# Performance work log

Hardware: AMD Instinct MI355X
Metric: run time of the kernel (lower is better)

The kernel has to match this reference:

```python
import jax, jax.numpy as jnp
import numpy as np

EPS = 1e-6
N_HEADS = 16
N_KV_HEADS = 4
HEAD_DIM = 128
DIM = 2048
SEQ = 2048
BATCH = 2


def _make_freqs_cis(seqlen, head_dim, theta=10000.0):
    inv = 1.0 / (theta ** (jnp.arange(0, head_dim, 2, dtype=jnp.float32) / head_dim))  # [hd/2]
    t = jnp.arange(seqlen, dtype=jnp.float32)
    ang = jnp.outer(t, inv)  # [seq, hd/2]
    return jnp.stack([jnp.cos(ang), jnp.sin(ang)], axis=-1)  # [seq, hd/2, 2]


def setup_inputs() -> dict:
    key = jax.random.key(0)
    k1, k2, k3 = jax.random.split(key, 3)
    std = 0.02
    x = jax.random.normal(k1, (BATCH, SEQ, DIM), dtype=jnp.float32)
    freqs_cis = _make_freqs_cis(SEQ, HEAD_DIM)
    norm_w = jnp.ones((DIM,), dtype=jnp.float32)
    wqkv_w = jax.random.normal(k2, ((N_HEADS + 2 * N_KV_HEADS) * HEAD_DIM, DIM), dtype=jnp.float32) * std
    wo_w = jax.random.normal(k3, (DIM, N_HEADS * HEAD_DIM), dtype=jnp.float32) * std
    return {"x": x, "freqs_cis": freqs_cis, "norm_w": norm_w, "wqkv_w": wqkv_w, "wo_w": wo_w}


def _rope(t, cos, sin):
    # t: [b, s, h, hd] viewed as pairs; cos/sin: [s, hd/2]
    b, s, h, hd = t.shape
    tr = t.reshape(b, s, h, hd // 2, 2)
    xr, xi = tr[..., 0], tr[..., 1]
    c = cos[None, :, None, :]
    sn = sin[None, :, None, :]
    out_r = xr * c - xi * sn
    out_i = xr * sn + xi * c
    return jnp.stack([out_r, out_i], axis=-1).reshape(b, s, h, hd)


def reference(x, freqs_cis, norm_w, wqkv_w, wo_w):
    bs, seqlen, dim = x.shape
    n_rep = N_HEADS // N_KV_HEADS
    # RMSNorm
    xn = x * jax.lax.rsqrt(jnp.mean(x * x, axis=-1, keepdims=True) + EPS) * norm_w
    # fused QKV projection
    qkv = jnp.einsum('bsd,ed->bse', xn, wqkv_w)
    q_sz = N_HEADS * HEAD_DIM
    kv_sz = N_KV_HEADS * HEAD_DIM
    xq = qkv[..., :q_sz].reshape(bs, seqlen, N_HEADS, HEAD_DIM)
    xk = qkv[..., q_sz:q_sz + kv_sz].reshape(bs, seqlen, N_KV_HEADS, HEAD_DIM)
    xv = qkv[..., q_sz + kv_sz:].reshape(bs, seqlen, N_KV_HEADS, HEAD_DIM)
    cos, sin = freqs_cis[..., 0], freqs_cis[..., 1]
    xq = _rope(xq, cos, sin)
    xk = _rope(xk, cos, sin)
    # GQA: group q heads so kv broadcast replaces repeat_kv materialization
    q = xq.transpose(0, 2, 1, 3).reshape(bs, N_KV_HEADS, n_rep, seqlen, HEAD_DIM)
    k = xk.transpose(0, 2, 1, 3)  # [b, g, s, d]
    v = xv.transpose(0, 2, 1, 3)
    scale = 1.0 / jnp.sqrt(jnp.float32(HEAD_DIM))
    scores = jnp.einsum('bgrqd,bgkd->bgrqk', q, k) * scale
    causal = jnp.tril(jnp.ones((seqlen, seqlen), dtype=bool))
    scores = jnp.where(causal, scores, jnp.finfo(scores.dtype).min)
    probs = jax.nn.softmax(scores, axis=-1)
    out = jnp.einsum('bgrqk,bgkd->bgrqd', probs, v)
    out = out.reshape(bs, N_HEADS, seqlen, HEAD_DIM).transpose(0, 2, 1, 3).reshape(bs, seqlen, N_HEADS * HEAD_DIM)
    return jnp.einsum('bse,de->bsd', out, wo_w)
```

## Files before the change

### kernel.cpp

```cpp
#include <hip/hip_runtime.h>
#include <cstdint>
#include <cstddef>

typedef __bf16 bhalf;
typedef __bf16 bhalf8 __attribute__((ext_vector_type(8)));
typedef __bf16 bhalf4 __attribute__((ext_vector_type(4)));
typedef float f32x4 __attribute__((ext_vector_type(4)));
typedef float f32x16 __attribute__((ext_vector_type(16)));

#define RMS_EPS 1e-6f
#define N_HEADS 16
#define N_KV 4
#define HD 128
#define DIM 2048
#define SEQ 2048
#define BATCH 2

static __device__ __forceinline__ f32x4 mfma16(bhalf8 a, bhalf8 b, f32x4 c) {
    return __builtin_amdgcn_mfma_f32_16x16x32_bf16(a, b, c, 0, 0, 0);
}
static __device__ __forceinline__ f32x16 mfma32(bhalf8 a, bhalf8 b, f32x16 c) {
    return __builtin_amdgcn_mfma_f32_32x32x16_bf16(a, b, c, 0, 0, 0);
}

static __device__ __forceinline__ void gload16(const bhalf* g, bhalf* l) {
    __builtin_amdgcn_global_load_lds((const __attribute__((address_space(1))) unsigned int*)g,
                                     (__attribute__((address_space(3))) unsigned int*)l,
                                     16, 0, 0);
}

static __device__ __forceinline__ unsigned cvt_pk_bf16(float a, float b) {
    unsigned r;
    asm volatile("v_cvt_pk_bf16_f32 %0, %1, %2" : "=v"(r) : "v"(a), "v"(b));
    return r;
}
static __device__ __forceinline__ void plane32_swap(unsigned& a, unsigned& b) {
    asm volatile("v_permlane32_swap_b32 %0, %1" : "+v"(a), "+v"(b));
}

__global__ __launch_bounds__(256) void cvt_w(const float* __restrict__ a,
                                             const float* __restrict__ b,
                                             bhalf* __restrict__ dst) {
    size_t i = ((size_t)blockIdx.x * 256 + threadIdx.x) * 4;
    const size_t NQ = (size_t)3072 * 2048;
    float4 v = (i < NQ) ? ((const float4*)a)[i >> 2] : ((const float4*)b)[(i - NQ) >> 2];
    bhalf4 o;
    o[0] = (bhalf)v.x; o[1] = (bhalf)v.y; o[2] = (bhalf)v.z; o[3] = (bhalf)v.w;
    *(bhalf4*)(dst + i) = o;
}

__global__ __launch_bounds__(256) void rmsnorm_k(const float* __restrict__ x,
                                                 const float* __restrict__ w,
                                                 bhalf* __restrict__ xn) {
    const int row = blockIdx.x;
    const int tid = threadIdx.x;
    const float4* xr = (const float4*)(x + (size_t)row * DIM);
    float4 v0 = xr[tid * 2], v1 = xr[tid * 2 + 1];
    float ss = v0.x * v0.x + v0.y * v0.y + v0.z * v0.z + v0.w * v0.w
             + v1.x * v1.x + v1.y * v1.y + v1.z * v1.z + v1.w * v1.w;
    #pragma unroll
    for (int off = 32; off; off >>= 1) ss += __shfl_xor(ss, off, 64);
    __shared__ float red[4];
    if ((tid & 63) == 0) red[tid >> 6] = ss;
    __syncthreads();
    float tot = red[0] + red[1] + red[2] + red[3];
    float scale = rsqrtf(tot * (1.0f / DIM) + RMS_EPS);
    const float4* wr = (const float4*)w;
    float4 w0 = wr[tid * 2], w1 = wr[tid * 2 + 1];
    bhalf8 o;
    o[0] = (bhalf)(v0.x * scale * w0.x); o[1] = (bhalf)(v0.y * scale * w0.y);
    o[2] = (bhalf)(v0.z * scale * w0.z); o[3] = (bhalf)(v0.w * scale * w0.w);
    o[4] = (bhalf)(v1.x * scale * w1.x); o[5] = (bhalf)(v1.y * scale * w1.y);
    o[6] = (bhalf)(v1.z * scale * w1.z); o[7] = (bhalf)(v1.w * scale * w1.w);
    *(bhalf8*)(xn + (size_t)row * DIM + tid * 8) = o;
}

template <typename OutT>
__global__ __launch_bounds__(512) void gemm8p(const bhalf* __restrict__ A,
                                              const bhalf* __restrict__ B,
                                              OutT* __restrict__ C,
                                              int N, int K) {
    extern __shared__ __align__(16) char smem[];
    const int tid = threadIdx.x;
    const int wid = tid >> 6, lane = tid & 63;
    const int quad = lane >> 4, r16 = lane & 15;
    const int wm = wid >> 2, wn = wid & 3;

    const int nx = N >> 8;
    const int cpx = (int)gridDim.x >> 3;
    const int bs = (int)blockIdx.x;
    const int bid = (bs & 7) * cpx + (bs >> 3);
    const int m0 = (bid / nx) << 8, n0 = (bid % nx) << 8;

    const int srow = wid * 8 + (lane >> 3);
    const int scol = ((lane & 7) ^ ((lane >> 3) & 7)) << 3;
    const bhalf* Asrc = A + (size_t)(m0 + srow) * K + scol;
    const bhalf* Bsrc = B + (size_t)(n0 + srow) * K + scol;
    const size_t r64K = (size_t)64 * K;
    const size_t r128K = (size_t)128 * K;

    const int x7 = r16 & 7;
    const int sl0 = (quad ^ (x7 & 3)) << 4;
    const int ksx = (x7 >> 2) << 6;
    const int k0 = ksx, k1 = 64 ^ ksx;
    const int aoff = (wm << 14) + (r16 << 7) + sl0;
    const int boff = ((2 + (wn >> 1)) << 14) + ((((wn & 1) << 6) + r16) << 7) + sl0;

    f32x4 acc[8][4];
    #pragma unroll
    for (int i = 0; i < 8; ++i)
        #pragma unroll
        for (int j = 0; j < 4; ++j) acc[i][j] = (f32x4)0.0f;

    const int NT = K >> 6;
    const int H = K >> 4;
    int h = 8;

    auto STAGE = [&](int hidx) {
        const int T = hidx >> 2, f = hidx & 3;
        const bhalf* s = ((f < 2) ? Asrc : Bsrc) + ((f & 1) ? r128K : 0) + T * 64;
        char* d = smem + ((T & 1) << 16) + (f << 14) + (wid << 10);
        gload16(s, (bhalf*)d);
        gload16(s + r64K, (bhalf*)(d + 8192));
    };

    #pragma unroll
    for (int i = 0; i < 8; ++i) STAGE(i);
    asm volatile("s_waitcnt vmcnt(8)" ::: "memory");
    __builtin_amdgcn_s_barrier();

    bhalf8 af[4][2], bf[4][2];

    for (int t = 0; t < NT; t += 2) {
        #pragma unroll
        for (int hf = 0; hf < 2; ++hf) {
            char* const bp = smem + (hf << 16);
            #pragma unroll
            for (int i = 0; i < 4; ++i) {
                af[i][0] = *(const bhalf8*)(bp + aoff + i * 2048 + k0);
                af[i][1] = *(const bhalf8*)(bp + aoff + i * 2048 + k1);
            }
            #pragma unroll
            for (int j = 0; j < 2; ++j) {
                bf[j][0] = *(const bhalf8*)(bp + boff + j * 2048 + k0);
                bf[j][1] = *(const bhalf8*)(bp + boff + j * 2048 + k1);
            }
            if ((t > 0 || hf == 1) && h < H) STAGE(h++);
            asm volatile("s_waitcnt lgkmcnt(8)" ::: "memory");
            __builtin_amdgcn_s_barrier();
            __builtin_amdgcn_s_setprio(1);
            #pragma unroll
            for (int i = 0; i < 4; ++i)
                #pragma unroll
                for (int j = 0; j < 2; ++j) {
                    acc[i][j] = mfma16(af[i][0], bf[j][0], acc[i][j]);
                    acc[i][j] = mfma16(af[i][1], bf[j][1], acc[i][j]);
                }
            __builtin_amdgcn_s_setprio(0);
            __builtin_amdgcn_s_barrier();

            #pragma unroll
            for (int j = 2; j < 4; ++j) {
                bf[j][0] = *(const bhalf8*)(bp + boff + j * 2048 + k0);
                bf[j][1] = *(const bhalf8*)(bp + boff + j * 2048 + k1);
            }
            if ((t > 0 || hf == 1) && h < H) STAGE(h++);
            __builtin_amdgcn_s_barrier();
            __builtin_amdgcn_s_setprio(1);
            #pragma unroll
            for (int i = 0; i < 4; ++i)
                #pragma unroll
                for (int j = 2; j < 4; ++j) {
                    acc[i][j] = mfma16(af[i][0], bf[j][0], acc[i][j]);
                    acc[i][j] = mfma16(af[i][1], bf[j][1], acc[i][j]);
                }
            __builtin_amdgcn_s_setprio(0);
            __builtin_amdgcn_s_barrier();

            #pragma unroll
            for (int i = 0; i < 4; ++i) {
                af[i][0] = *(const bhalf8*)(bp + aoff + (i + 4) * 2048 + k0);
                af[i][1] = *(const bhalf8*)(bp + aoff + (i + 4) * 2048 + k1);
            }
            if ((t > 0 || hf == 1) && h < H) STAGE(h++);
            __builtin_amdgcn_s_barrier();
            __builtin_amdgcn_s_setprio(1);
            #pragma unroll
            for (int i = 0; i < 4; ++i)
                #pragma unroll
                for (int j = 0; j < 2; ++j) {
                    acc[i + 4][j] = mfma16(af[i][0], bf[j][0], acc[i + 4][j]);
                    acc[i + 4][j] = mfma16(af[i][1], bf[j][1], acc[i + 4][j]);
                }
            __builtin_amdgcn_s_setprio(0);
            __builtin_amdgcn_s_barrier();

            bool st = (h < H);
            if (st) STAGE(h++);
            __builtin_amdgcn_s_barrier();
            __builtin_amdgcn_s_setprio(1);
            #pragma unroll
            for (int i = 0; i < 4; ++i)
                #pragma unroll
                for (int j = 2; j < 4; ++j) {
                    acc[i + 4][j] = mfma16(af[i][0], bf[j][0], acc[i + 4][j]);
                    acc[i + 4][j] = mfma16(af[i][1], bf[j][1], acc[i + 4][j]);
                }
            __builtin_amdgcn_s_setprio(0);
            if (st) asm volatile("s_waitcnt vmcnt(2)" ::: "memory");
            else    asm volatile("s_waitcnt vmcnt(0)" ::: "memory");
            __builtin_amdgcn_s_barrier();
        }
    }

    #pragma unroll
    for (int i = 0; i < 8; ++i) {
        const int rbase = m0 + wm * 128 + i * 16 + quad * 4;
        #pragma unroll
        for (int rr = 0; rr < 4; ++rr) {
            OutT* crow = C + (size_t)(rbase + rr) * N + n0 + wn * 64 + r16;
            #pragma unroll
            for (int j = 0; j < 4; ++j) crow[j * 16] = (OutT)acc[i][j][rr];
        }
    }
}

__global__ __launch_bounds__(256) void rope_k(const bhalf* __restrict__ qkv,
                                              const float* __restrict__ freqs,
                                              bhalf* __restrict__ qb,
                                              bhalf* __restrict__ kb,
                                              bhalf* __restrict__ vt) {
    const int bs = blockIdx.x;
    const int b = bs >> 11, s = bs & 2047;
    const bhalf* row = qkv + (size_t)bs * 3072;
    const int tid = threadIdx.x;

    {
        const int h = tid >> 4, d20 = (tid & 15) * 4;
        bhalf8 e = *(const bhalf8*)(row + h * HD + d20 * 2);
        const float* fp = freqs + (size_t)s * 128 + d20 * 2;
        float4 f0 = *(const float4*)fp;
        float4 f1 = *(const float4*)(fp + 4);
        bhalf8 o;
        o[0] = (bhalf)((float)e[0] * f0.x - (float)e[1] * f0.y);
        o[1] = (bhalf)((float)e[0] * f0.y + (float)e[1] * f0.x);
        o[2] = (bhalf)((float)e[2] * f0.z - (float)e[3] * f0.w);
        o[3] = (bhalf)((float)e[2] * f0.w + (float)e[3] * f0.z);
        o[4] = (bhalf)((float)e[4] * f1.x - (float)e[5] * f1.y);
        o[5] = (bhalf)((float)e[4] * f1.y + (float)e[5] * f1.x);
        o[6] = (bhalf)((float)e[6] * f1.z - (float)e[7] * f1.w);
        o[7] = (bhalf)((float)e[6] * f1.w + (float)e[7] * f1.z);
        *(bhalf8*)(qb + ((size_t)(b * N_HEADS + h) * SEQ + s) * HD + d20 * 2) = o;
    }
    if (tid < 64) {
        const int kh = tid >> 4, d20 = (tid & 15) * 4;
        bhalf8 e = *(const bhalf8*)(row + 2048 + kh * HD + d20 * 2);
        const float* fp = freqs + (size_t)s * 128 + d20 * 2;
        float4 f0 = *(const float4*)fp;
        float4 f1 = *(const float4*)(fp + 4);
        bhalf8 o;
        o[0] = (bhalf)((float)e[0] * f0.x - (float)e[1] * f0.y);
        o[1] = (bhalf)((float)e[0] * f0.y + (float)e[1] * f0.x);
        o[2] = (bhalf)((float)e[2] * f0.z - (float)e[3] * f0.w);
        o[3] = (bhalf)((float)e[2] * f0.w + (float)e[3] * f0.z);
        o[4] = (bhalf)((float)e[4] * f1.x - (float)e[5] * f1.y);
        o[5] = (bhalf)((float)e[4] * f1.y + (float)e[5] * f1.x);
        o[6] = (bhalf)((float)e[6] * f1.z - (float)e[7] * f1.w);
        o[7] = (bhalf)((float)e[6] * f1.w + (float)e[7] * f1.z);
        *(bhalf8*)(kb + ((size_t)(b * N_KV + kh) * SEQ + s) * HD + d20 * 2) = o;
    }
    for (int e = tid; e < 512; e += 256) {
        const int kh = e >> 7, d = e & 127;
        vt[((size_t)(b * N_KV + kh) * HD + d) * SEQ + s] = row[2560 + e];
    }
}

__global__ __launch_bounds__(256, 2) void attn_k(const bhalf* __restrict__ qb,
                                                 const bhalf* __restrict__ kb,
                                                 const bhalf* __restrict__ vt,
                                                 bhalf* __restrict__ ob) {
    const int tid = threadIdx.x;
    const int wave = tid >> 6, lane = tid & 63;
    const int l31 = lane & 31, h2 = lane >> 5;
    const int qw = wave & 1, kw = wave >> 1;
    const int bid = ((blockIdx.x & 7) << 6) | ((int)blockIdx.x >> 3);
    const int pair = bid & 15;
    const int hh = (bid >> 4) & 15;
    const int b = bid >> 8;
    const int kvh = hh >> 2;

    __shared__ __align__(16) char smem[33792];
    char* const sK = smem;
    char* const sV = smem + 16384;
    float* const mrg = (float*)smem;

    const bhalf* Kbase = kb + (size_t)(b * N_KV + kvh) * SEQ * HD;
    const bhalf* Vbase = vt + (size_t)(b * N_KV + kvh) * HD * SEQ;
    const float SCL2 = 0.08838834764831845f * 1.4426950408889634f;

    const int mbase = (qw * 64 + lane) * 66;
    const int kr = tid >> 4, kce = (tid & 15) * 8;
    const int vr = tid >> 3, vce = (tid & 7) * 8;
    const int kcB = kce * 2, vcB = vce * 2;
    const int Xl = (h2 << 4) ^ ((l31 & 7) << 4);

    for (int phase = 0; phase < 2; ++phase) {
        const int qt = phase ? (31 - pair) : pair;
        const int qrow = qt * 64 + qw * 32 + l31;
        const int qhi = qt * 64 + qw * 32 + 31;

        const bhalf* qbase = qb + (((size_t)(b * N_HEADS + hh) * SEQ) + qrow) * HD;
        bhalf8 qf[8];
        #pragma unroll
        for (int kk = 0; kk < 8; ++kk) {
            bhalf8 q0 = *(const bhalf8*)(qbase + kk * 16 + h2 * 8);
            #pragma unroll
            for (int e = 0; e < 8; ++e) q0[e] = (bhalf)((float)q0[e] * SCL2);
            qf[kk] = q0;
        }

        f32x16 accO[4];
        #pragma unroll
        for (int dt = 0; dt < 4; ++dt) accO[dt] = (f32x16)0.0f;
        float m_i = -1e30f, l_i = 0.0f;

        bhalf8 kreg[4], vreg[4];
        #pragma unroll
        for (int i = 0; i < 4; ++i) {
            kreg[i] = *(const bhalf8*)(Kbase + (size_t)(kr + 16 * i) * HD + kce);
            vreg[i] = *(const bhalf8*)(Vbase + (size_t)(vr + 32 * i) * SEQ + vce);
        }

        for (int kt = 0; kt <= qt; ++kt) {
            __syncthreads();
            #pragma unroll
            for (int i = 0; i < 4; ++i) {
                const int rk = kr + 16 * i;
                *(bhalf8*)(sK + rk * 256 + (kcB ^ ((rk & 7) << 4))) = kreg[i];
                const int rv = vr + 32 * i;
                *(bhalf8*)(sV + rv * 128 + (vcB ^ ((rv & 7) << 4))) = vreg[i];
            }
            __syncthreads();
            if (kt < qt) {
                const int kn = (kt + 1) * 64;
                #pragma unroll
                for (int i = 0; i < 4; ++i) {
                    kreg[i] = *(const bhalf8*)(Kbase + (size_t)(kn + kr + 16 * i) * HD + kce);
                    vreg[i] = *(const bhalf8*)(Vbase + (size_t)(vr + 32 * i) * SEQ + kn + vce);
                }
            }
            if (qhi < kt * 64 + kw * 32) continue;

            f32x16 accS = (f32x16)0.0f;
            const char* kRow = sK + (kw * 32 + l31) * 256;
            #pragma unroll
            for (int kk = 0; kk < 8; ++kk)
                accS = mfma32(*(const bhalf8*)(kRow + ((kk * 32) ^ Xl)), qf[kk], accS);

            if (kt == qt) {
                #pragma unroll
                for (int r = 0; r < 16; ++r) {
                    const int key = kt * 64 + kw * 32 + (r & 3) + 8 * (r >> 2) + 4 * h2;
                    if (key > qrow) accS[r] = -1e30f;
                }
            }

            float mx = -1e30f;
            #pragma unroll
            for (int r = 0; r < 16; ++r) mx = fmaxf(mx, accS[r]);
            mx = fmaxf(mx, __shfl_xor(mx, 32, 64));

            if (!__all(mx <= m_i + 8.0f)) {
                const float mnew = fmaxf(m_i, mx);
                const float alpha = __builtin_amdgcn_exp2f(m_i - mnew);
                m_i = mnew;
                l_i *= alpha;
                #pragma unroll
                for (int dt = 0; dt < 4; ++dt)
                    #pragma unroll
                    for (int r = 0; r < 16; ++r) accO[dt][r] *= alpha;
            }

            float p[16];
            float rs = 0.0f;
            #pragma unroll
            for (int r = 0; r < 16; ++r) {
                p[r] = __builtin_amdgcn_exp2f(accS[r] - m_i);
                rs += p[r];
            }
            rs += __shfl_xor(rs, 32, 64);
            l_i += rs;

            unsigned X0 = cvt_pk_bf16(p[0],  p[1]);
            unsigned X1 = cvt_pk_bf16(p[2],  p[3]);
            unsigned X2 = cvt_pk_bf16(p[4],  p[5]);
            unsigned X3 = cvt_pk_bf16(p[6],  p[7]);
            unsigned X4 = cvt_pk_bf16(p[8],  p[9]);
            unsigned X5 = cvt_pk_bf16(p[10], p[11]);
            unsigned X6 = cvt_pk_bf16(p[12], p[13]);
            unsigned X7 = cvt_pk_bf16(p[14], p[15]);
            plane32_swap(X0, X2);
            plane32_swap(X1, X3);
            plane32_swap(X4, X6);
            plane32_swap(X5, X7);
            union { unsigned u[8]; bhalf8 h[2]; } pk;
            pk.u[0] = X0; pk.u[1] = X1; pk.u[2] = X2; pk.u[3] = X3;
            pk.u[4] = X4; pk.u[5] = X5; pk.u[6] = X6; pk.u[7] = X7;

            #pragma unroll
            for (int kk2 = 0; kk2 < 2; ++kk2) {
                const int cb = (kw << 6) | (kk2 << 5);
                #pragma unroll
                for (int dt = 0; dt < 4; ++dt) {
                    const bhalf8 vfv = *(const bhalf8*)(sV + (dt * 32 + l31) * 128 + (cb ^ Xl));
                    accO[dt] = mfma32(vfv, pk.h[kk2], accO[dt]);
                }
            }
        }

        __syncthreads();
        if (kw == 1) {
            #pragma unroll
            for (int dt = 0; dt < 4; ++dt)
                #pragma unroll
                for (int r = 0; r < 16; ++r) mrg[mbase + dt * 16 + r] = accO[dt][r];
            mrg[mbase + 64] = m_i;
            mrg[mbase + 65] = l_i;
        }
        __syncthreads();
        if (kw == 0) {
            const float m1 = mrg[mbase + 64];
            const float l1 = mrg[mbase + 65];
            const float m = fmaxf(m_i, m1);
            const float b0 = __builtin_amdgcn_exp2f(m_i - m);
            const float b1 = __builtin_amdgcn_exp2f(m1 - m);
            const float inv = 1.0f / (l_i * b0 + l1 * b1);
            bhalf* obase = ob + ((size_t)b * SEQ + qrow) * (size_t)(N_HEADS * HD) + hh * HD;
            #pragma unroll
            for (int dt = 0; dt < 4; ++dt)
                #pragma unroll
                for (int c = 0; c < 4; ++c) {
                    bhalf4 o4;
                    #pragma unroll
                    for (int rr = 0; rr < 4; ++rr) {
                        const float v = accO[dt][c * 4 + rr] * b0 +
                                        mrg[mbase + dt * 16 + c * 4 + rr] * b1;
                        o4[rr] = (bhalf)(v * inv);
                    }
                    *(bhalf4*)(obase + dt * 32 + c * 8 + h2 * 4) = o4;
                }
        }
    }
}

extern "C" void kernel_launch(void* const* d_in, const int* in_sizes, int n_in,
                              void* d_out, int out_size, void* d_ws, size_t ws_size,
                              hipStream_t stream) {
    const float* x      = (const float*)d_in[0];
    const float* freqs  = (const float*)d_in[1];
    const float* norm_w = (const float*)d_in[2];
    const float* wqkv   = (const float*)d_in[3];
    const float* wo     = (const float*)d_in[4];
    float* out = (float*)d_out;

    char* ws = (char*)d_ws;
    bhalf* wqkv_b = (bhalf*)(ws);
    bhalf* wo_b   = (bhalf*)(ws + 12582912);
    bhalf* xn     = (bhalf*)(ws + 20971520);
    bhalf* qkv    = (bhalf*)(ws + 37748736);
    bhalf* qb     = (bhalf*)(ws + 88080384);
    bhalf* kb     = (bhalf*)(ws + 104857600);
    bhalf* vtb    = (bhalf*)(ws + 109051904);
    bhalf* attn   = (bhalf*)(ws + 113246208);

    static bool attr_done = false;
    if (!attr_done) {
        hipFuncSetAttribute((const void*)gemm8p<bhalf>,
                            hipFuncAttributeMaxDynamicSharedMemorySize, 131072);
        hipFuncSetAttribute((const void*)gemm8p<float>,
                            hipFuncAttributeMaxDynamicSharedMemorySize, 131072);
        attr_done = true;
    }

    cvt_w<<<10240, 256, 0, stream>>>(wqkv, wo, wqkv_b);
    rmsnorm_k<<<BATCH * SEQ, 256, 0, stream>>>(x, norm_w, xn);
    gemm8p<bhalf><<<192, 512, 131072, stream>>>(xn, wqkv_b, qkv, 3072, 2048);
    rope_k<<<BATCH * SEQ, 256, 0, stream>>>(qkv, freqs, qb, kb, vtb);
    attn_k<<<512, 256, 0, stream>>>(qb, kb, vtb, attn);
    gemm8p<float><<<128, 512, 131072, stream>>>(attn, wo_b, out, 2048, 2048);
}
```

Baseline: 316.1 us.

## Add 128x128 tile GEMM for output projection and separate LDS V transpose

```diff
diff --git a/kernel.cpp b/kernel.cpp
--- a/kernel.cpp
+++ b/kernel.cpp
@@ -225,11 +225,99 @@
     }
 }
 
+template <typename OutT>
+__global__ __launch_bounds__(256) void gemm128(const bhalf* __restrict__ A,
+                                               const bhalf* __restrict__ B,
+                                               OutT* __restrict__ C,
+                                               int N, int K) {
+    const int tid = threadIdx.x;
+    const int w = tid >> 6, lane = tid & 63;
+    const int quad = lane >> 4, r16 = lane & 15;
+    const int wm = w >> 1, wn = w & 1;
+
+    const int nx = N >> 7;
+    const int cpx = (int)gridDim.x >> 3;
+    const int bs = (int)blockIdx.x;
+    const int bid = (bs & 7) * cpx + (bs >> 3);
+    const int m0 = (bid / nx) << 7, n0 = (bid % nx) << 7;
+
+    __shared__ __align__(16) char smem[49152];
+    char* const sA = smem;
+    char* const sB = smem + 24576;
+
+    const int srow = lane >> 2;
+    const int scol = ((lane & 3) ^ (srow & 3)) << 3;
+    const bhalf* Ast = A + (size_t)(m0 + w * 16 + srow) * K + scol;
+    const bhalf* Bst = B + (size_t)(n0 + w * 16 + srow) * K + scol;
+    const size_t r64K = (size_t)64 * K;
+
+    const int xorr = (r16 & 3) << 4;
+    const int rdA = (wm * 64 + r16) * 64 + ((quad * 16) ^ xorr);
+    const int rdB = (wn * 64 + r16) * 64 + ((quad * 16) ^ xorr);
+
+    f32x4 acc[4][4];
+    #pragma unroll
+    for (int i = 0; i < 4; ++i)
+        #pragma unroll
+        for (int j = 0; j < 4; ++j) acc[i][j] = (f32x4)0.0f;
+
+    const int NT = K >> 5;
+
+    #define STG128(t, buf) do {                                                        \
+        gload16(Ast + (size_t)(t) * 32,        (bhalf*)(sA + (buf) * 8192 + w * 1024));        \
+        gload16(Ast + (size_t)(t) * 32 + r64K, (bhalf*)(sA + (buf) * 8192 + 4096 + w * 1024)); \
+        gload16(Bst + (size_t)(t) * 32,        (bhalf*)(sB + (buf) * 8192 + w * 1024));        \
+        gload16(Bst + (size_t)(t) * 32 + r64K, (bhalf*)(sB + (buf) * 8192 + 4096 + w * 1024)); \
+    } while (0)
+
+    STG128(0, 0);
+    STG128(1, 1);
+
+    int cur = 0, c2 = 2;
+    for (int t = 0; t < NT; ++t) {
+        if (t + 1 < NT) asm volatile("s_waitcnt vmcnt(4)" ::: "memory");
+        else            asm volatile("s_waitcnt vmcnt(0)" ::: "memory");
+        __builtin_amdgcn_s_barrier();
+
+        char* const bufA = sA + cur * 8192;
+        char* const bufB = sB + cur * 8192;
+        bhalf8 af[4], bf[4];
+        #pragma unroll
+        for (int i = 0; i < 4; ++i) af[i] = *(const bhalf8*)(bufA + rdA + i * 1024);
+        #pragma unroll
+        for (int j = 0; j < 4; ++j) bf[j] = *(const bhalf8*)(bufB + rdB + j * 1024);
+
+        if (t + 2 < NT) STG128(t + 2, c2);
+
+        __builtin_amdgcn_s_setprio(1);
+        #pragma unroll
+        for (int i = 0; i < 4; ++i)
+            #pragma unroll
+            for (int j = 0; j < 4; ++j)
+                acc[i][j] = mfma16(af[i], bf[j], acc[i][j]);
+        __builtin_amdgcn_s_setprio(0);
+
+        cur = (cur == 2) ? 0 : cur + 1;
+        c2 = (c2 == 2) ? 0 : c2 + 1;
+    }
+    #undef STG128
+
+    #pragma unroll
+    for (int i = 0; i < 4; ++i) {
+        const int rbase = m0 + wm * 64 + i * 16 + quad * 4;
+        #pragma unroll
+        for (int rr = 0; rr < 4; ++rr) {
+            OutT* crow = C + (size_t)(rbase + rr) * N + n0 + wn * 64 + r16;
+            #pragma unroll
+            for (int j = 0; j < 4; ++j) crow[j * 16] = (OutT)acc[i][j][rr];
+        }
+    }
+}
+
 __global__ __launch_bounds__(256) void rope_k(const bhalf* __restrict__ qkv,
                                               const float* __restrict__ freqs,
                                               bhalf* __restrict__ qb,
-                                              bhalf* __restrict__ kb,
-                                              bhalf* __restrict__ vt) {
+                                              bhalf* __restrict__ kb) {
     const int bs = blockIdx.x;
     const int b = bs >> 11, s = bs & 2047;
     const bhalf* row = qkv + (size_t)bs * 3072;
@@ -269,9 +357,40 @@
         o[7] = (bhalf)((float)e[6] * f1.w + (float)e[7] * f1.z);
         *(bhalf8*)(kb + ((size_t)(b * N_KV + kh) * SEQ + s) * HD + d20 * 2) = o;
     }
-    for (int e = tid; e < 512; e += 256) {
-        const int kh = e >> 7, d = e & 127;
-        vt[((size_t)(b * N_KV + kh) * HD + d) * SEQ + s] = row[2560 + e];
+}
+
+__global__ __launch_bounds__(256) void vtrans_k(const bhalf* __restrict__ qkv,
+                                                bhalf* __restrict__ vt) {
+    const int blk = blockIdx.x;
+    const int sc = blk & 31;
+    const int kvh = (blk >> 5) & 3;
+    const int b = blk >> 7;
+    const int s0 = sc * 64;
+    const int tid = threadIdx.x;
+    __shared__ __align__(16) char lds[64 * 256];
+
+    const int rr = tid >> 4;
+    const int slot = tid & 15;
+    #pragma unroll
+    for (int p = 0; p < 4; ++p) {
+        const int s = p * 16 + rr;
+        bhalf8 v = *(const bhalf8*)(qkv + (size_t)(b * SEQ + s0 + s) * 3072
+                                    + 2560 + kvh * HD + slot * 8);
+        *(bhalf8*)(lds + s * 256 + ((slot ^ ((s >> 3) & 7)) << 4)) = v;
+    }
+    __syncthreads();
+    const int j = tid & 7;
+    const int d0 = tid >> 3;
+    #pragma unroll
+    for (int p = 0; p < 4; ++p) {
+        const int d = p * 32 + d0;
+        bhalf8 o;
+        #pragma unroll
+        for (int e = 0; e < 8; ++e) {
+            const int s = j * 8 + e;
+            o[e] = *(const bhalf*)(lds + s * 256 + (((d >> 3) ^ j) << 4) + (d & 7) * 2);
+        }
+        *(bhalf8*)(vt + ((size_t)(b * N_KV + kvh) * HD + d) * SEQ + s0 + j * 8) = o;
     }
 }
 
@@ -477,15 +596,14 @@
     if (!attr_done) {
         hipFuncSetAttribute((const void*)gemm8p<bhalf>,
                             hipFuncAttributeMaxDynamicSharedMemorySize, 131072);
-        hipFuncSetAttribute((const void*)gemm8p<float>,
-                            hipFuncAttributeMaxDynamicSharedMemorySize, 131072);
         attr_done = true;
     }
 
     cvt_w<<<10240, 256, 0, stream>>>(wqkv, wo, wqkv_b);
     rmsnorm_k<<<BATCH * SEQ, 256, 0, stream>>>(x, norm_w, xn);
     gemm8p<bhalf><<<192, 512, 131072, stream>>>(xn, wqkv_b, qkv, 3072, 2048);
-    rope_k<<<BATCH * SEQ, 256, 0, stream>>>(qkv, freqs, qb, kb, vtb);
+    rope_k<<<BATCH * SEQ, 256, 0, stream>>>(qkv, freqs, qb, kb);
+    vtrans_k<<<256, 256, 0, stream>>>(qkv, vtb);
     attn_k<<<512, 256, 0, stream>>>(qb, kb, vtb, attn);
-    gemm8p<float><<<128, 512, 131072, stream>>>(attn, wo_b, out, 2048, 2048);
-}
+    gemm128<float><<<512, 256, 0, stream>>>(attn, wo_b, out, 2048, 2048);
+}
```

Result: faster. 290.8 us (-8.0%).
